# Kernel tuning notes

Hardware: AMD Instinct MI355X
Metric: run time of the kernel (lower is better)

Reference implementation:

```python
import jax, jax.numpy as jnp
import numpy as np

B, S = 4096, 8192

def setup_inputs() -> dict:
    key = jax.random.key(0)
    k1, k2, k3 = jax.random.split(key, 3)
    scores = jax.random.normal(k1, (B, S, 1), dtype=jnp.float32)
    label = jax.random.randint(k2, (B,), 0, 2).astype(jnp.float32)
    # seqlen in [16, 8192) so k = seqlen//16 + 1 is always <= seqlen
    seqlen = jax.random.randint(k3, (B,), 16, S, dtype=jnp.int32)
    return {"scores": scores, "label": label, "seqlen": seqlen}


def reference(scores, label, seqlen):
    # scores: [B, S, 1] -> [B, S]; per-row variable-length top-k mean (k = seqlen//16 + 1),
    # then sigmoid + BCE vs label. Vectorized via mask + descending sort + prefix mask.
    s = scores.squeeze(-1)                                   # [B, S]
    pos = jnp.arange(s.shape[1])                             # [S]
    valid = pos[None, :] < seqlen[:, None]                   # [B, S] ragged mask
    masked = jnp.where(valid, s, -jnp.inf)
    desc = -jnp.sort(-masked, axis=-1)                       # descending sort per row
    k = seqlen // 16 + 1                                     # _cfg.k == -1 branch
    topk_mask = pos[None, :] < k[:, None]                    # first k sorted entries
    topk_mean = jnp.sum(jnp.where(topk_mask, desc, 0.0), axis=-1) / k.astype(s.dtype)
    inst = jax.nn.sigmoid(topk_mean)                         # [B]
    # nn.BCELoss (mean reduction)
    eps = 1e-12
    loss = -jnp.mean(label * jnp.log(inst + eps) + (1.0 - label) * jnp.log(1.0 - inst + eps))
    return loss
```

## Files before the change

kernel.cpp:

```cpp
#include <hip/hip_runtime.h>
#include <stdint.h>


#define SLEN 8192
#define BLK 256
#define NB 4096
#define CAP 4096
#define LOV (-6.0f)
#define SCALE (NB / 12.0f)

__device__ __forceinline__ int bin_of(float x) {
  float t = (x - LOV) * SCALE;
  int b = (int)t;
  b = b < 0 ? 0 : (b > NB - 1 ? NB - 1 : b);
  return b;
}

__global__ __launch_bounds__(BLK) void topk_bce_rows(
    const float* __restrict__ scores, const float* __restrict__ label,
    const int* __restrict__ seqlen, float* __restrict__ rowterm) {
  __shared__ uint32_t hist[NB];
  __shared__ uint32_t wtot[4];
  __shared__ uint32_t selBin, selAbove;
  __shared__ int ccount;
  __shared__ float redbuf[4];

  const int row = blockIdx.x;
  const int tid = threadIdx.x;
  const int lane = tid & 63;
  const int wave = tid >> 6;
  const int n = seqlen[row];
  const uint32_t k = (uint32_t)(n >> 4) + 1;

  #pragma unroll
  for (int i = 0; i < NB / BLK; ++i) hist[i * BLK + tid] = 0u;
  if (tid == 0) ccount = 0;

  const float4* src = reinterpret_cast<const float4*>(scores + (size_t)row * SLEN);
  float v[32];
  #pragma unroll
  for (int i = 0; i < 8; ++i) {
    float4 q = src[i * BLK + tid];
    v[i * 4 + 0] = q.x; v[i * 4 + 1] = q.y;
    v[i * 4 + 2] = q.z; v[i * 4 + 3] = q.w;
  }
  __syncthreads();

  #pragma unroll
  for (int i = 0; i < 8; ++i) {
    #pragma unroll
    for (int c = 0; c < 4; ++c) {
      int pos = i * 1024 + tid * 4 + c;
      if (pos < n) {
        int b = bin_of(v[i * 4 + c]);
        atomicAdd(&hist[((b & 15) << 8) | (b >> 4)], 1u);
      }
    }
  }
  __syncthreads();

  uint32_t wsum = 0;
  #pragma unroll
  for (int i = 0; i < 16; ++i) wsum += hist[(i << 8) + tid];

  uint32_t sfx = wsum;
  #pragma unroll
  for (int d = 1; d < 64; d <<= 1) {
    uint32_t o = __shfl_down(sfx, d, 64);
    if (lane + d < 64) sfx += o;
  }
  if (lane == 0) wtot[wave] = sfx;
  __syncthreads();
  uint32_t tail_w = 0;
  for (int w = wave + 1; w < 4; ++w) tail_w += wtot[w];
  const uint32_t sfx_all = sfx + tail_w;
  const uint32_t tail = sfx_all - wsum;

  uint32_t acc = tail;
  #pragma unroll
  for (int i = 15; i >= 0; --i) {
    uint32_t h = hist[(i << 8) + tid];
    uint32_t acc2 = acc + h;
    if (acc2 >= k && acc < k) { selBin = (uint32_t)((tid << 4) | i); selAbove = acc; }
    acc = acc2;
  }
  __syncthreads();
  const int bstar = (int)selBin;
  const uint32_t remaining = k - selAbove;

  float* cand = (float*)hist;
  float psum = 0.0f;
  #pragma unroll
  for (int i = 0; i < 8; ++i) {
    #pragma unroll
    for (int c = 0; c < 4; ++c) {
      int pos = i * 1024 + tid * 4 + c;
      if (pos < n) {
        float x = v[i * 4 + c];
        int b = bin_of(x);
        if (b > bstar) {
          psum += x;
        } else if (b == bstar) {
          int idx = atomicAdd(&ccount, 1);
          if (idx < CAP) cand[idx] = x;
        }
      }
    }
  }
  __syncthreads();
  const int C = min(ccount, CAP);

  for (int i = tid; i < C; i += BLK) {
    float x = cand[i];
    uint32_t r = 0;
    for (int j = 0; j < C; ++j) {
      float y = cand[j];
      r += (uint32_t)((y > x) || (y == x && j < i));
    }
    if (r < remaining) psum += x;
  }

  #pragma unroll
  for (int d = 32; d >= 1; d >>= 1) psum += __shfl_down(psum, d, 64);
  if (lane == 0) redbuf[wave] = psum;
  __syncthreads();
  if (tid == 0) {
    float tot = redbuf[0] + redbuf[1] + redbuf[2] + redbuf[3];
    float mean = tot / (float)k;
    float inst = 1.0f / (1.0f + expf(-mean));
    float lab = label[row];
    float term = lab * logf(inst + 1e-12f) +
                 (1.0f - lab) * logf(1.0f - inst + 1e-12f);
    rowterm[row] = term;
  }
}

__global__ __launch_bounds__(BLK) void reduce_rows(
    const float* __restrict__ rowterm, float* __restrict__ out, int rows) {
  __shared__ float red[4];
  const int tid = threadIdx.x;
  const int lane = tid & 63;
  const int wave = tid >> 6;
  float s = 0.0f;
  for (int i = tid; i < rows; i += BLK) s += rowterm[i];
  #pragma unroll
  for (int d = 32; d >= 1; d >>= 1) s += __shfl_down(s, d, 64);
  if (lane == 0) red[wave] = s;
  __syncthreads();
  if (tid == 0) out[0] = -(red[0] + red[1] + red[2] + red[3]) / (float)rows;
}

extern "C" void kernel_launch(void* const* d_in, const int* in_sizes, int n_in,
                              void* d_out, int out_size, void* d_ws, size_t ws_size,
                              hipStream_t stream) {
  const float* scores = (const float*)d_in[0];
  const float* label  = (const float*)d_in[1];
  const int*   seqlen = (const int*)d_in[2];
  float* out = (float*)d_out;
  float* rowterm = (float*)d_ws;

  const int rows = in_sizes[1];

  topk_bce_rows<<<rows, BLK, 0, stream>>>(scores, label, seqlen, rowterm);
  reduce_rows<<<1, BLK, 0, stream>>>(rowterm, out, rows);
}
```

Baseline: 200.4 us.

## Shrink histogram to one bin per thread with 512-thread blocks

Doubles the block size to 512 threads and cuts the radix histogram from 4096 to 512 bins, so each thread owns exactly one bin. The bin-select step becomes a single block-wide suffix scan instead of a 16-bin-per-thread strided pass. Candidates get their own small shared buffer, and the final reduce kernel uses 1024 threads. This is meant to cut shared-memory zeroing, scanning and footprint, and to raise occupancy. The cost is wider bins: more candidates land in the threshold bin, and the quadratic rank pass plus the risk of overflowing the 1024-entry candidate cap both grow.

```diff
diff --git a/kernel.cpp b/kernel.cpp
--- a/kernel.cpp
+++ b/kernel.cpp
@@ -3,9 +3,11 @@
 
 
 #define SLEN 8192
-#define BLK 256
-#define NB 4096
-#define CAP 4096
+#define BLK 512
+#define NWAVE (BLK / 64)
+#define VPT (SLEN / BLK / 4)
+#define NB 512
+#define CAP 1024
 #define LOV (-6.0f)
 #define SCALE (NB / 12.0f)
 
@@ -16,14 +18,15 @@
   return b;
 }
 
-__global__ __launch_bounds__(BLK) void topk_bce_rows(
+__global__ __launch_bounds__(BLK, 6) void topk_bce_rows(
     const float* __restrict__ scores, const float* __restrict__ label,
     const int* __restrict__ seqlen, float* __restrict__ rowterm) {
   __shared__ uint32_t hist[NB];
-  __shared__ uint32_t wtot[4];
+  __shared__ float cand[CAP];
+  __shared__ uint32_t wtot[NWAVE];
   __shared__ uint32_t selBin, selAbove;
   __shared__ int ccount;
-  __shared__ float redbuf[4];
+  __shared__ float redbuf[NWAVE];
 
   const int row = blockIdx.x;
   const int tid = threadIdx.x;
@@ -32,37 +35,30 @@
   const int n = seqlen[row];
   const uint32_t k = (uint32_t)(n >> 4) + 1;
 
+  const float4* src = reinterpret_cast<const float4*>(scores + (size_t)row * SLEN);
+  float v[VPT * 4];
   #pragma unroll
-  for (int i = 0; i < NB / BLK; ++i) hist[i * BLK + tid] = 0u;
-  if (tid == 0) ccount = 0;
-
-  const float4* src = reinterpret_cast<const float4*>(scores + (size_t)row * SLEN);
-  float v[32];
-  #pragma unroll
-  for (int i = 0; i < 8; ++i) {
+  for (int i = 0; i < VPT; ++i) {
     float4 q = src[i * BLK + tid];
     v[i * 4 + 0] = q.x; v[i * 4 + 1] = q.y;
     v[i * 4 + 2] = q.z; v[i * 4 + 3] = q.w;
   }
+
+  hist[tid] = 0u;
+  if (tid == 0) ccount = 0;
   __syncthreads();
 
   #pragma unroll
-  for (int i = 0; i < 8; ++i) {
+  for (int i = 0; i < VPT; ++i) {
     #pragma unroll
     for (int c = 0; c < 4; ++c) {
-      int pos = i * 1024 + tid * 4 + c;
-      if (pos < n) {
-        int b = bin_of(v[i * 4 + c]);
-        atomicAdd(&hist[((b & 15) << 8) | (b >> 4)], 1u);
-      }
+      int pos = i * (BLK * 4) + tid * 4 + c;
+      if (pos < n) atomicAdd(&hist[bin_of(v[i * 4 + c])], 1u);
     }
   }
   __syncthreads();
 
-  uint32_t wsum = 0;
-  #pragma unroll
-  for (int i = 0; i < 16; ++i) wsum += hist[(i << 8) + tid];
-
+  const uint32_t wsum = hist[tid];
   uint32_t sfx = wsum;
   #pragma unroll
   for (int d = 1; d < 64; d <<= 1) {
@@ -71,30 +67,23 @@
   }
   if (lane == 0) wtot[wave] = sfx;
   __syncthreads();
-  uint32_t tail_w = 0;
-  for (int w = wave + 1; w < 4; ++w) tail_w += wtot[w];
-  const uint32_t sfx_all = sfx + tail_w;
-  const uint32_t tail = sfx_all - wsum;
-
-  uint32_t acc = tail;
+  uint32_t tailw = 0;
   #pragma unroll
-  for (int i = 15; i >= 0; --i) {
-    uint32_t h = hist[(i << 8) + tid];
-    uint32_t acc2 = acc + h;
-    if (acc2 >= k && acc < k) { selBin = (uint32_t)((tid << 4) | i); selAbove = acc; }
-    acc = acc2;
-  }
+  for (int w = 0; w < NWAVE; ++w)
+    if (w > wave) tailw += wtot[w];
+  const uint32_t F = sfx + tailw;
+  const uint32_t above = F - wsum;
+  if (F >= k && above < k) { selBin = (uint32_t)tid; selAbove = above; }
   __syncthreads();
   const int bstar = (int)selBin;
   const uint32_t remaining = k - selAbove;
 
-  float* cand = (float*)hist;
   float psum = 0.0f;
   #pragma unroll
-  for (int i = 0; i < 8; ++i) {
+  for (int i = 0; i < VPT; ++i) {
     #pragma unroll
     for (int c = 0; c < 4; ++c) {
-      int pos = i * 1024 + tid * 4 + c;
+      int pos = i * (BLK * 4) + tid * 4 + c;
       if (pos < n) {
         float x = v[i * 4 + c];
         int b = bin_of(x);
@@ -125,7 +114,9 @@
   if (lane == 0) redbuf[wave] = psum;
   __syncthreads();
   if (tid == 0) {
-    float tot = redbuf[0] + redbuf[1] + redbuf[2] + redbuf[3];
+    float tot = 0.0f;
+    #pragma unroll
+    for (int w = 0; w < NWAVE; ++w) tot += redbuf[w];
     float mean = tot / (float)k;
     float inst = 1.0f / (1.0f + expf(-mean));
     float lab = label[row];
@@ -135,19 +126,24 @@
   }
 }
 
-__global__ __launch_bounds__(BLK) void reduce_rows(
+__global__ __launch_bounds__(1024) void reduce_rows(
     const float* __restrict__ rowterm, float* __restrict__ out, int rows) {
-  __shared__ float red[4];
+  __shared__ float red[16];
   const int tid = threadIdx.x;
   const int lane = tid & 63;
   const int wave = tid >> 6;
   float s = 0.0f;
-  for (int i = tid; i < rows; i += BLK) s += rowterm[i];
+  for (int i = tid; i < rows; i += 1024) s += rowterm[i];
   #pragma unroll
   for (int d = 32; d >= 1; d >>= 1) s += __shfl_down(s, d, 64);
   if (lane == 0) red[wave] = s;
   __syncthreads();
-  if (tid == 0) out[0] = -(red[0] + red[1] + red[2] + red[3]) / (float)rows;
+  if (tid == 0) {
+    float tot = 0.0f;
+    #pragma unroll
+    for (int w = 0; w < 16; ++w) tot += red[w];
+    out[0] = -tot / (float)rows;
+  }
 }
 
 extern "C" void kernel_launch(void* const* d_in, const int* in_sizes, int n_in,
@@ -162,5 +158,5 @@
   const int rows = in_sizes[1];
 
   topk_bce_rows<<<rows, BLK, 0, stream>>>(scores, label, seqlen, rowterm);
-  reduce_rows<<<1, BLK, 0, stream>>>(rowterm, out, rows);
+  reduce_rows<<<1, 1024, 0, stream>>>(rowterm, out, rows);
 }
```

Measured after the change: 192.7 us. 3.9% less time.
